# Kernel optimization log

Hardware: AMD Instinct MI355X
Metric: run time of the kernel (lower is better)

Reference implementation:

```python
import jax, jax.numpy as jnp
import numpy as np

B, H, S, D = 4, 16, 1024, 64
TEMPERATURE = 8.0  # sqrt(D)


def setup_inputs() -> dict:
    key = jax.random.key(0)
    k1, k2, k3, k4, k5, k6 = jax.random.split(key, 6)
    return {
        "q": jax.random.normal(k1, (B, H, S, D), dtype=jnp.float32),
        "k": jax.random.normal(k2, (B, H, S, D), dtype=jnp.float32),
        "v": jax.random.normal(k3, (B, H, S, D), dtype=jnp.float32),
        "mask": jax.random.randint(k4, (B, 1, 1, S), 0, 2, dtype=jnp.int32),
        "adj_matrix": jax.random.normal(k5, (B, S, S), dtype=jnp.float32),
        "dist_matrix": jax.random.uniform(k6, (B, S, S), dtype=jnp.float32),
    }


def reference(q, k, v, mask, adj_matrix, dist_matrix):
    # attn = (q / temperature) @ k^T  -> [B,H,S,S]
    attn = jnp.einsum("bhqd,bhkd->bhqk", q / TEMPERATURE, k)

    # distance-based rescaling: (1 + e) / (1 + exp(1 - dist)), broadcast over heads
    dist = dist_matrix[:, None, :, :]  # [B,1,S,S]
    one = jnp.float32(1.0)
    rescaled = (one + jnp.exp(one)) / (one + jnp.exp(one - dist))
    attn = jax.nn.relu(attn) * rescaled

    # additive adjacency bias, broadcast over heads
    attn = attn + adj_matrix[:, None, :, :]

    # mask fill
    attn = jnp.where(mask == 0, jnp.float32(-1e9), attn)

    attn = jax.nn.softmax(attn, axis=-1)  # dropout p used in eval -> identity
    output = jnp.einsum("bhqk,bhkd->bhqd", attn, v)
    return (output, attn)
```

## Files before the change

### kernel.cpp

```cpp
#include <hip/hip_runtime.h>
#include <hip/hip_bf16.h>

#define NB 4
#define NH 16
#define NS 1024
#define ND 64

typedef __bf16 bf16x8 __attribute__((ext_vector_type(8)));
typedef float f32x4 __attribute__((ext_vector_type(4)));
typedef unsigned short u16x8 __attribute__((ext_vector_type(8)));

__device__ __forceinline__ void split_bf16(const float* f, bf16x8& hi, bf16x8& lo) {
#pragma unroll
    for (int j = 0; j < 8; ++j) {
        float x = f[j];
        __bf16 h = (__bf16)x;
        hi[j] = h;
        lo[j] = (__bf16)(x - (float)h);
    }
}

__global__ __launch_bounds__(256) void fused_attn_kernel(
    const float* __restrict__ Q, const float* __restrict__ K, const float* __restrict__ V,
    const int* __restrict__ mask, const float* __restrict__ adj, const float* __restrict__ dist,
    float* __restrict__ out_g, float* __restrict__ attn_g)
{
    const int tid  = (int)threadIdx.x;
    const int lane = tid & 63;
    const int wid  = tid >> 6;
    const int qi   = lane & 15;
    const int g    = lane >> 4;

    const int bid = (int)blockIdx.x;
    const int qt  = bid & 63;
    const int bh  = bid >> 6;
    const int b   = bh >> 4;

    __shared__ __align__(16) unsigned short Plds[4][16 * 256];
    __shared__ __align__(16) float outp[4][16][68];
    __shared__ float red_m[4][16];
    __shared__ float red_l[4][16];

    const int qglob = qt * 16 + qi;
    const int kw    = wid * 256;

    bf16x8 qh[2], ql[2];
    {
        const float* qp = Q + (bh * NS + qglob) * ND + g * 8;
#pragma unroll
        for (int c = 0; c < 2; ++c) {
            f32x4 f0 = *(const f32x4*)(qp + c * 32);
            f32x4 f1 = *(const f32x4*)(qp + c * 32 + 4);
            float f[8];
#pragma unroll
            for (int j = 0; j < 4; ++j) { f[j] = f0[j] * 0.125f; f[j + 4] = f1[j] * 0.125f; }
            split_bf16(f, qh[c], ql[c]);
        }
    }

    f32x4 acc[16];
    {
        const f32x4 z = {0.f, 0.f, 0.f, 0.f};
#pragma unroll
        for (int t = 0; t < 16; ++t) acc[t] = z;
    }
#pragma unroll
    for (int t = 0; t < 16; ++t) {
        const float* kp = K + (bh * NS + kw + t * 16 + qi) * ND + g * 8;
#pragma unroll
        for (int c = 0; c < 2; ++c) {
            f32x4 f0 = *(const f32x4*)(kp + c * 32);
            f32x4 f1 = *(const f32x4*)(kp + c * 32 + 4);
            float f[8];
#pragma unroll
            for (int j = 0; j < 4; ++j) { f[j] = f0[j]; f[j + 4] = f1[j]; }
            bf16x8 kh, kl;
            split_bf16(f, kh, kl);
            acc[t] = __builtin_amdgcn_mfma_f32_16x16x32_bf16(kh, qh[c], acc[t], 0, 0, 0);
            acc[t] = __builtin_amdgcn_mfma_f32_16x16x32_bf16(kl, qh[c], acc[t], 0, 0, 0);
            acc[t] = __builtin_amdgcn_mfma_f32_16x16x32_bf16(kh, ql[c], acc[t], 0, 0, 0);
        }
    }

    const float* adjR  = adj  + (b * NS + qglob) * NS;
    const float* distR = dist + (b * NS + qglob) * NS;
    const int*   maskR = mask + b * NS;
    const float  CE = 3.7182817f;

#pragma unroll
    for (int t = 0; t < 16; ++t) {
        const int k0 = kw + t * 16 + g * 4;
        f32x4 a4 = *(const f32x4*)(adjR + k0);
        f32x4 d4 = *(const f32x4*)(distR + k0);
        int4  m4 = *(const int4*)(maskR + k0);
        int   mm[4] = {m4.x, m4.y, m4.z, m4.w};
#pragma unroll
        for (int r = 0; r < 4; ++r) {
            float s = fmaxf(acc[t][r], 0.f);
            float resc = CE * __builtin_amdgcn_rcpf(1.f + __expf(1.f - d4[r]));
            s = s * resc + a4[r];
            acc[t][r] = (mm[r] == 0) ? -1.0e9f : s;
        }
    }

    float m = -3.0e38f;
#pragma unroll
    for (int t = 0; t < 16; ++t)
#pragma unroll
        for (int r = 0; r < 4; ++r) m = fmaxf(m, acc[t][r]);
    m = fmaxf(m, __shfl_xor(m, 16, 64));
    m = fmaxf(m, __shfl_xor(m, 32, 64));
    if (g == 0) red_m[wid][qi] = m;
    __syncthreads();
    const float mf = fmaxf(fmaxf(red_m[0][qi], red_m[1][qi]),
                           fmaxf(red_m[2][qi], red_m[3][qi]));

    float l = 0.f;
#pragma unroll
    for (int t = 0; t < 16; ++t)
#pragma unroll
        for (int r = 0; r < 4; ++r) {
            float e = __expf(acc[t][r] - mf);
            acc[t][r] = e;
            l += e;
        }
    l += __shfl_xor(l, 16, 64);
    l += __shfl_xor(l, 32, 64);
    if (g == 0) red_l[wid][qi] = l;
    __syncthreads();
    const float lf = red_l[0][qi] + red_l[1][qi] + red_l[2][qi] + red_l[3][qi];
    const float inv = __builtin_amdgcn_rcpf(lf);

    float* attnR = attn_g + (bh * NS + qglob) * NS;
    unsigned short* Pw = &Plds[wid][0];
#pragma unroll
    for (int t = 0; t < 16; ++t) {
        const int kloc = t * 16 + g * 4;
        f32x4 e4;
#pragma unroll
        for (int r = 0; r < 4; ++r) e4[r] = acc[t][r] * inv;
        __builtin_nontemporal_store(e4, (f32x4*)(attnR + kw + kloc));

        unsigned int p01 = ((unsigned int)__builtin_bit_cast(unsigned short, (__bf16)e4[0]))
                         | ((unsigned int)__builtin_bit_cast(unsigned short, (__bf16)e4[1]) << 16);
        unsigned int p23 = ((unsigned int)__builtin_bit_cast(unsigned short, (__bf16)e4[2]))
                         | ((unsigned int)__builtin_bit_cast(unsigned short, (__bf16)e4[3]) << 16);
        const int u = kloc >> 2;
        const int c = u >> 1;
        unsigned long long pk = (unsigned long long)p01 | ((unsigned long long)p23 << 32);
        *(unsigned long long*)((char*)Pw + qi * 512 + ((c ^ (qi & 7)) << 4) + (u & 1) * 8) = pk;
    }
    __syncthreads();

    f32x4 o[4];
    {
        const f32x4 z = {0.f, 0.f, 0.f, 0.f};
#pragma unroll
        for (int dt = 0; dt < 4; ++dt) o[dt] = z;
    }
    const float* vbase = V + (bh * NS + kw) * ND;
#pragma unroll
    for (int j = 0; j < 8; ++j) {
        const int c = j * 4 + g;
        const u16x8 praw = *(const u16x8*)((const char*)Pw + qi * 512 + ((c ^ (qi & 7)) << 4));
        const bf16x8 pa = __builtin_bit_cast(bf16x8, praw);
        const float* vp0 = vbase + (j * 32 + g * 8) * ND + qi;
#pragma unroll
        for (int dt = 0; dt < 4; ++dt) {
            bf16x8 vb;
            const float* vp = vp0 + dt * 16;
#pragma unroll
            for (int r = 0; r < 8; ++r) vb[r] = (__bf16)vp[r * ND];
            o[dt] = __builtin_amdgcn_mfma_f32_16x16x32_bf16(pa, vb, o[dt], 0, 0, 0);
        }
    }

#pragma unroll
    for (int dt = 0; dt < 4; ++dt)
#pragma unroll
        for (int r = 0; r < 4; ++r)
            outp[wid][g * 4 + r][dt * 16 + qi] = o[dt][r];
    __syncthreads();
    {
        const int qrow = tid >> 4;
        const int d0   = (tid & 15) * 4;
        f32x4 s = *(const f32x4*)(&outp[0][qrow][d0]);
#pragma unroll
        for (int w = 1; w < 4; ++w) s += *(const f32x4*)(&outp[w][qrow][d0]);
        __builtin_nontemporal_store(s, (f32x4*)(out_g + (bh * NS + qt * 16 + qrow) * ND + d0));
    }
}

extern "C" void kernel_launch(void* const* d_in, const int* in_sizes, int n_in,
                              void* d_out, int out_size, void* d_ws, size_t ws_size,
                              hipStream_t stream) {
    const float* Q    = (const float*)d_in[0];
    const float* K    = (const float*)d_in[1];
    const float* V    = (const float*)d_in[2];
    const int*   mask = (const int*)d_in[3];
    const float* adj  = (const float*)d_in[4];
    const float* dist = (const float*)d_in[5];
    float* out  = (float*)d_out;
    float* attn = out + (size_t)NB * NH * NS * ND;

    dim3 grid(NB * NH * (NS / 16));
    fused_attn_kernel<<<grid, 256, 0, stream>>>(Q, K, V, mask, adj, dist, out, attn);
}
```

Measured before the change: 579.4 us.

## Precompute bf16 hi/lo Q,K and transposed bf16 V in workspace before fused attention

Adds pre-pass kernels that split Q (pre-scaled) and K into bf16 hi/lo halves and write V as a transposed bf16 array in workspace. The main kernel then loads packed bf16 vectors instead of converting fp32 on every one of the 64 query-tile blocks that reread K and V per head. It also reuses one shared-memory buffer for P and the output reduction, and swizzles the block order. The cost is three extra launches and an extra pass over Q, K and V through workspace. The old kernel remains as a fallback when the workspace is too small.

```diff
diff --git a/kernel.cpp b/kernel.cpp
--- a/kernel.cpp
+++ b/kernel.cpp
@@ -5,18 +5,212 @@
 #define NH 16
 #define NS 1024
 #define ND 64
+#define NBH (NB * NH)
+#define NELEM ((size_t)NBH * NS * ND)
 
 typedef __bf16 bf16x8 __attribute__((ext_vector_type(8)));
 typedef float f32x4 __attribute__((ext_vector_type(4)));
 typedef unsigned short u16x8 __attribute__((ext_vector_type(8)));
-
-__device__ __forceinline__ void split_bf16(const float* f, bf16x8& hi, bf16x8& lo) {
+typedef unsigned short u16x4 __attribute__((ext_vector_type(4)));
+
+
+__global__ __launch_bounds__(256) void conv_hilo(const float* __restrict__ src,
+                                                 unsigned short* __restrict__ hi,
+                                                 unsigned short* __restrict__ lo,
+                                                 float scale, int n4) {
+    int i = blockIdx.x * 256 + threadIdx.x;
+    if (i >= n4) return;
+    f32x4 x = ((const f32x4*)src)[i];
+    u16x4 h, l;
+#pragma unroll
+    for (int j = 0; j < 4; ++j) {
+        float xs = x[j] * scale;
+        __bf16 hb = (__bf16)xs;
+        h[j] = __builtin_bit_cast(unsigned short, hb);
+        l[j] = __builtin_bit_cast(unsigned short, (__bf16)(xs - (float)hb));
+    }
+    ((u16x4*)hi)[i] = h;
+    ((u16x4*)lo)[i] = l;
+}
+
+__global__ __launch_bounds__(256) void conv_vt(const float* __restrict__ V,
+                                               unsigned short* __restrict__ Vt) {
+    int i = blockIdx.x * 256 + threadIdx.x;
+    int bh = i >> 12;
+    int kb = (i >> 6) & 63;
+    int d  = i & 63;
+    const float* vp = V + ((size_t)(bh * NS + kb * 16)) * ND + d;
+    unsigned short* op = Vt + ((size_t)(bh * ND + d)) * NS + kb * 16;
+    u16x8 o0, o1;
+#pragma unroll
+    for (int r = 0; r < 8; ++r) o0[r] = __builtin_bit_cast(unsigned short, (__bf16)vp[r * ND]);
+#pragma unroll
+    for (int r = 0; r < 8; ++r) o1[r] = __builtin_bit_cast(unsigned short, (__bf16)vp[(r + 8) * ND]);
+    *(u16x8*)op = o0;
+    *(u16x8*)(op + 8) = o1;
+}
+
+__global__ __launch_bounds__(256) void fused_attn_pre(
+    const unsigned short* __restrict__ Qhi, const unsigned short* __restrict__ Qlo,
+    const unsigned short* __restrict__ Khi, const unsigned short* __restrict__ Klo,
+    const unsigned short* __restrict__ Vt,
+    const int* __restrict__ mask, const float* __restrict__ adj, const float* __restrict__ dist,
+    float* __restrict__ out_g, float* __restrict__ attn_g)
+{
+    const int tid  = (int)threadIdx.x;
+    const int lane = tid & 63;
+    const int wid  = tid >> 6;
+    const int qi   = lane & 15;
+    const int g    = lane >> 4;
+
+    int bid = (int)blockIdx.x;
+    bid = (bid & 7) * (NBH * 64 / 8) + (bid >> 3);
+    const int qt = bid & 63;
+    const int bh = bid >> 6;
+    const int b  = bh >> 4;
+
+    __shared__ __align__(16) unsigned char smem[4 * 16 * 256 * 2 + 512];
+    unsigned short* Plds = (unsigned short*)smem;
+    float* red_m = (float*)(smem + 32768);
+    float* red_l = red_m + 64;
+    typedef float outp_t[16][68];
+    outp_t* outp = (outp_t*)smem;
+
+    const int qglob = qt * 16 + qi;
+    const int kw    = wid * 256;
+
+    bf16x8 qh[2], ql[2];
+    {
+        const size_t qo = ((size_t)(bh * NS + qglob)) * ND + g * 8;
+        qh[0] = __builtin_bit_cast(bf16x8, *(const u16x8*)(Qhi + qo));
+        qh[1] = __builtin_bit_cast(bf16x8, *(const u16x8*)(Qhi + qo + 32));
+        ql[0] = __builtin_bit_cast(bf16x8, *(const u16x8*)(Qlo + qo));
+        ql[1] = __builtin_bit_cast(bf16x8, *(const u16x8*)(Qlo + qo + 32));
+    }
+
+    f32x4 acc[16];
+    {
+        const f32x4 z = {0.f, 0.f, 0.f, 0.f};
+#pragma unroll
+        for (int t = 0; t < 16; ++t) acc[t] = z;
+    }
+#pragma unroll
+    for (int t = 0; t < 16; ++t) {
+        const size_t ko = ((size_t)(bh * NS + kw + t * 16 + qi)) * ND + g * 8;
+#pragma unroll
+        for (int c = 0; c < 2; ++c) {
+            bf16x8 kh = __builtin_bit_cast(bf16x8, *(const u16x8*)(Khi + ko + c * 32));
+            bf16x8 kl = __builtin_bit_cast(bf16x8, *(const u16x8*)(Klo + ko + c * 32));
+            acc[t] = __builtin_amdgcn_mfma_f32_16x16x32_bf16(kh, qh[c], acc[t], 0, 0, 0);
+            acc[t] = __builtin_amdgcn_mfma_f32_16x16x32_bf16(kl, qh[c], acc[t], 0, 0, 0);
+            acc[t] = __builtin_amdgcn_mfma_f32_16x16x32_bf16(kh, ql[c], acc[t], 0, 0, 0);
+        }
+    }
+
+    const float* adjR  = adj  + ((size_t)(b * NS + qglob)) * NS;
+    const float* distR = dist + ((size_t)(b * NS + qglob)) * NS;
+    const int*   maskR = mask + b * NS;
+    const float  CE = 3.7182817f;
+
+#pragma unroll
+    for (int t = 0; t < 16; ++t) {
+        const int k0 = kw + t * 16 + g * 4;
+        f32x4 a4 = *(const f32x4*)(adjR + k0);
+        f32x4 d4 = *(const f32x4*)(distR + k0);
+        int4  m4 = *(const int4*)(maskR + k0);
+        int   mm[4] = {m4.x, m4.y, m4.z, m4.w};
+#pragma unroll
+        for (int r = 0; r < 4; ++r) {
+            float s = fmaxf(acc[t][r], 0.f);
+            float resc = CE * __builtin_amdgcn_rcpf(1.f + __expf(1.f - d4[r]));
+            s = s * resc + a4[r];
+            acc[t][r] = (mm[r] == 0) ? -1.0e9f : s;
+        }
+    }
+
+    float m = -3.0e38f;
+#pragma unroll
+    for (int t = 0; t < 16; ++t)
+#pragma unroll
+        for (int r = 0; r < 4; ++r) m = fmaxf(m, acc[t][r]);
+    m = fmaxf(m, __shfl_xor(m, 16, 64));
+    m = fmaxf(m, __shfl_xor(m, 32, 64));
+    if (g == 0) red_m[wid * 16 + qi] = m;
+    __syncthreads();
+    const float mf = fmaxf(fmaxf(red_m[qi], red_m[16 + qi]),
+                           fmaxf(red_m[32 + qi], red_m[48 + qi]));
+
+    float l = 0.f;
+#pragma unroll
+    for (int t = 0; t < 16; ++t)
+#pragma unroll
+        for (int r = 0; r < 4; ++r) {
+            float e = __expf(acc[t][r] - mf);
+            acc[t][r] = e;
+            l += e;
+        }
+    l += __shfl_xor(l, 16, 64);
+    l += __shfl_xor(l, 32, 64);
+    if (g == 0) red_l[wid * 16 + qi] = l;
+    __syncthreads();
+    const float lf = red_l[qi] + red_l[16 + qi] + red_l[32 + qi] + red_l[48 + qi];
+    const float inv = __builtin_amdgcn_rcpf(lf);
+
+    float* attnR = attn_g + ((size_t)(bh * NS + qglob)) * NS;
+    unsigned short* Pw = Plds + wid * (16 * 256);
+#pragma unroll
+    for (int t = 0; t < 16; ++t) {
+        const int kloc = t * 16 + g * 4;
+        f32x4 e4;
+#pragma unroll
+        for (int r = 0; r < 4; ++r) e4[r] = acc[t][r] * inv;
+        __builtin_nontemporal_store(e4, (f32x4*)(attnR + kw + kloc));
+
+        unsigned int p01 = ((unsigned int)__builtin_bit_cast(unsigned short, (__bf16)e4[0]))
+                         | ((unsigned int)__builtin_bit_cast(unsigned short, (__bf16)e4[1]) << 16);
+        unsigned int p23 = ((unsigned int)__builtin_bit_cast(unsigned short, (__bf16)e4[2]))
+                         | ((unsigned int)__builtin_bit_cast(unsigned short, (__bf16)e4[3]) << 16);
+        const int u = kloc >> 2;
+        const int c = u >> 1;
+        unsigned long long pk = (unsigned long long)p01 | ((unsigned long long)p23 << 32);
+        *(unsigned long long*)((char*)Pw + qi * 512 + ((c ^ (qi & 7)) << 4) + (u & 1) * 8) = pk;
+    }
+    __syncthreads();
+
+    f32x4 o[4];
+    {
+        const f32x4 z = {0.f, 0.f, 0.f, 0.f};
+#pragma unroll
+        for (int dt = 0; dt < 4; ++dt) o[dt] = z;
+    }
+    const unsigned short* vtb = Vt + ((size_t)bh * ND) * NS;
 #pragma unroll
     for (int j = 0; j < 8; ++j) {
-        float x = f[j];
-        __bf16 h = (__bf16)x;
-        hi[j] = h;
-        lo[j] = (__bf16)(x - (float)h);
+        const int c = j * 4 + g;
+        const u16x8 praw = *(const u16x8*)((const char*)Pw + qi * 512 + ((c ^ (qi & 7)) << 4));
+        const bf16x8 pa = __builtin_bit_cast(bf16x8, praw);
+#pragma unroll
+        for (int dt = 0; dt < 4; ++dt) {
+            const bf16x8 vb = __builtin_bit_cast(bf16x8,
+                *(const u16x8*)(vtb + (size_t)(dt * 16 + qi) * NS + kw + j * 32 + g * 8));
+            o[dt] = __builtin_amdgcn_mfma_f32_16x16x32_bf16(pa, vb, o[dt], 0, 0, 0);
+        }
+    }
+    __syncthreads();
+
+#pragma unroll
+    for (int dt = 0; dt < 4; ++dt)
+#pragma unroll
+        for (int r = 0; r < 4; ++r)
+            outp[wid][g * 4 + r][dt * 16 + qi] = o[dt][r];
+    __syncthreads();
+    {
+        const int qrow = tid >> 4;
+        const int d0   = (tid & 15) * 4;
+        f32x4 s = *(const f32x4*)(&outp[0][qrow][d0]);
+#pragma unroll
+        for (int w = 1; w < 4; ++w) s += *(const f32x4*)(&outp[w][qrow][d0]);
+        __builtin_nontemporal_store(s, (f32x4*)(out_g + ((size_t)(bh * NS + qt * 16 + qrow)) * ND + d0));
     }
 }
 
@@ -51,10 +245,15 @@
         for (int c = 0; c < 2; ++c) {
             f32x4 f0 = *(const f32x4*)(qp + c * 32);
             f32x4 f1 = *(const f32x4*)(qp + c * 32 + 4);
-            float f[8];
-#pragma unroll
-            for (int j = 0; j < 4; ++j) { f[j] = f0[j] * 0.125f; f[j + 4] = f1[j] * 0.125f; }
-            split_bf16(f, qh[c], ql[c]);
+#pragma unroll
+            for (int j = 0; j < 4; ++j) {
+                float xh = f0[j] * 0.125f;
+                __bf16 hb = (__bf16)xh;
+                qh[c][j] = hb; ql[c][j] = (__bf16)(xh - (float)hb);
+                float xl = f1[j] * 0.125f;
+                __bf16 hb2 = (__bf16)xl;
+                qh[c][j + 4] = hb2; ql[c][j + 4] = (__bf16)(xl - (float)hb2);
+            }
         }
     }
 
@@ -71,19 +270,22 @@
         for (int c = 0; c < 2; ++c) {
             f32x4 f0 = *(const f32x4*)(kp + c * 32);
             f32x4 f1 = *(const f32x4*)(kp + c * 32 + 4);
-            float f[8];
-#pragma unroll
-            for (int j = 0; j < 4; ++j) { f[j] = f0[j]; f[j + 4] = f1[j]; }
             bf16x8 kh, kl;
-            split_bf16(f, kh, kl);
+#pragma unroll
+            for (int j = 0; j < 4; ++j) {
+                __bf16 hb = (__bf16)f0[j];
+                kh[j] = hb; kl[j] = (__bf16)(f0[j] - (float)hb);
+                __bf16 hb2 = (__bf16)f1[j];
+                kh[j + 4] = hb2; kl[j + 4] = (__bf16)(f1[j] - (float)hb2);
+            }
             acc[t] = __builtin_amdgcn_mfma_f32_16x16x32_bf16(kh, qh[c], acc[t], 0, 0, 0);
             acc[t] = __builtin_amdgcn_mfma_f32_16x16x32_bf16(kl, qh[c], acc[t], 0, 0, 0);
             acc[t] = __builtin_amdgcn_mfma_f32_16x16x32_bf16(kh, ql[c], acc[t], 0, 0, 0);
         }
     }
 
-    const float* adjR  = adj  + (b * NS + qglob) * NS;
-    const float* distR = dist + (b * NS + qglob) * NS;
+    const float* adjR  = adj  + (b * NS + qglob) * (size_t)NS;
+    const float* distR = dist + (b * NS + qglob) * (size_t)NS;
     const int*   maskR = mask + b * NS;
     const float  CE = 3.7182817f;
 
@@ -131,7 +333,7 @@
     const float lf = red_l[0][qi] + red_l[1][qi] + red_l[2][qi] + red_l[3][qi];
     const float inv = __builtin_amdgcn_rcpf(lf);
 
-    float* attnR = attn_g + (bh * NS + qglob) * NS;
+    float* attnR = attn_g + (bh * NS + qglob) * (size_t)NS;
     unsigned short* Pw = &Plds[wid][0];
 #pragma unroll
     for (int t = 0; t < 16; ++t) {
@@ -158,7 +360,7 @@
 #pragma unroll
         for (int dt = 0; dt < 4; ++dt) o[dt] = z;
     }
-    const float* vbase = V + (bh * NS + kw) * ND;
+    const float* vbase = V + (bh * NS + kw) * (size_t)ND;
 #pragma unroll
     for (int j = 0; j < 8; ++j) {
         const int c = j * 4 + g;
@@ -187,7 +389,7 @@
         f32x4 s = *(const f32x4*)(&outp[0][qrow][d0]);
 #pragma unroll
         for (int w = 1; w < 4; ++w) s += *(const f32x4*)(&outp[w][qrow][d0]);
-        __builtin_nontemporal_store(s, (f32x4*)(out_g + (bh * NS + qt * 16 + qrow) * ND + d0));
+        __builtin_nontemporal_store(s, (f32x4*)(out_g + (bh * NS + qt * 16 + qrow) * (size_t)ND + d0));
     }
 }
 
@@ -201,8 +403,22 @@
     const float* adj  = (const float*)d_in[4];
     const float* dist = (const float*)d_in[5];
     float* out  = (float*)d_out;
-    float* attn = out + (size_t)NB * NH * NS * ND;
-
-    dim3 grid(NB * NH * (NS / 16));
-    fused_attn_kernel<<<grid, 256, 0, stream>>>(Q, K, V, mask, adj, dist, out, attn);
+    float* attn = out + NELEM;
+
+    const size_t need = NELEM * 2 * 5;
+    if (ws_size >= need) {
+        unsigned short* Qhi = (unsigned short*)d_ws;
+        unsigned short* Qlo = Qhi + NELEM;
+        unsigned short* Khi = Qlo + NELEM;
+        unsigned short* Klo = Khi + NELEM;
+        unsigned short* Vt  = Klo + NELEM;
+        const int n4 = (int)(NELEM / 4);
+        conv_hilo<<<dim3(n4 / 256), 256, 0, stream>>>(Q, Qhi, Qlo, 0.125f, n4);
+        conv_hilo<<<dim3(n4 / 256), 256, 0, stream>>>(K, Khi, Klo, 1.0f, n4);
+        conv_vt<<<dim3(NBH * ND * (NS / 16) / 256), 256, 0, stream>>>(V, Vt);
+        fused_attn_pre<<<dim3(NBH * 64), 256, 0, stream>>>(Qhi, Qlo, Khi, Klo, Vt,
+                                                           mask, adj, dist, out, attn);
+    } else {
+        fused_attn_kernel<<<dim3(NBH * 64), 256, 0, stream>>>(Q, K, V, mask, adj, dist, out, attn);
+    }
 }
```

New measurement: 587.7 us. Within noise of the previous version (+1.4%).
